# Kernel tuning notes

Measured on AMD Instinct MI355X. Metric: run time of the kernel, lower is better.

## Reference

```python
import jax, jax.numpy as jnp
import numpy as np

NUM_HEADS = 8
KERNEL_SEARCH = 5  # local attention window
EPS = 1e-5


def _layernorm(x, g, b):
    m = jnp.mean(x, axis=-1, keepdims=True)
    v = jnp.var(x, axis=-1, keepdims=True)
    return (x - m) / jnp.sqrt(v + EPS) * g + b


def _unfold3(x):
    # x: [N, C, H, W] -> [N, C*9, H*W]; matches torch F.unfold(kernel=3, pad=1)
    # ordering: channel-major, kernel position (row-major) minor.
    N, C, H, W = x.shape
    xp = jnp.pad(x, ((0, 0), (0, 0), (1, 1), (1, 1)))
    pats = jnp.stack([xp[:, :, i:i + H, j:j + W] for i in range(3) for j in range(3)], axis=2)
    return pats.reshape(N, C * 9, H * W)


def _sai2token(x, w_mlp):
    # x: [b, c, a, h, w] -> tokens [h*w, b*a, spa_dim]
    b, c, a, h, w = x.shape
    x = x.transpose(0, 2, 1, 3, 4).reshape(b * a, c, h, w)
    tok = _unfold3(x).transpose(2, 0, 1)  # [hw, b*a, c*9]
    return jnp.einsum('lnk,ek->lne', tok, w_mlp)


def _local_mask(h, w, k):
    # additive mask [h*w, h*w]: 0 inside local kxk window, -inf outside
    kl, kr = k // 2, k - k // 2
    ii = jnp.arange(h)
    jj = jnp.arange(w)
    okh = (ii[None, :] >= ii[:, None] - kl) & (ii[None, :] < ii[:, None] + kr)  # [h,h]
    okw = (jj[None, :] >= jj[:, None] - kl) & (jj[None, :] < jj[:, None] + kr)  # [w,w]
    ok = okh[:, None, :, None] & okw[None, :, None, :]  # [h,w,h,w]
    ok = ok.reshape(h * w, h * w)
    return jnp.where(ok, 0.0, -jnp.inf).astype(jnp.float32)


def _attention(qk_in, v_in, in_proj_w, out_proj_w, bias):
    # qk_in/v_in: [L, B, E]; torch nn.MultiheadAttention, no biases, eval mode
    L, B, E = qk_in.shape
    Dh = E // NUM_HEADS
    Wq, Wk, Wv = in_proj_w[:E], in_proj_w[E:2 * E], in_proj_w[2 * E:]
    q = jnp.einsum('lbe,fe->lbf', qk_in, Wq).reshape(L, B, NUM_HEADS, Dh)
    k = jnp.einsum('lbe,fe->lbf', qk_in, Wk).reshape(L, B, NUM_HEADS, Dh)
    v = jnp.einsum('lbe,fe->lbf', v_in, Wv).reshape(L, B, NUM_HEADS, Dh)
    scale = 1.0 / np.sqrt(Dh).astype(np.float32)
    scores = jnp.einsum('lbhd,mbhd->bhlm', q, k) * scale + bias[None, None]
    attn = jax.nn.softmax(scores, axis=-1)
    out = jnp.einsum('bhlm,mbhd->lbhd', attn, v).reshape(L, B, E)
    return jnp.einsum('lbe,fe->lbf', out, out_proj_w)


def reference(buffer, spa_position, w_mlp, ln1_g, ln1_b, in_proj_w, out_proj_w,
              ln2_g, ln2_b, ff_w1, ff_w2, conv_w):
    b, c, a, h, w = buffer.shape
    bias = _local_mask(h, w, KERNEL_SEARCH)
    tok = _sai2token(buffer, w_mlp)          # [hw, b*a, E]
    pe = _sai2token(spa_position, w_mlp)
    x = _layernorm(tok + pe, ln1_g, ln1_b)
    tok = _attention(x, tok, in_proj_w, out_proj_w, bias) + tok
    # feed-forward (dropout is identity in eval)
    ff = _layernorm(tok, ln2_g, ln2_b)
    ff = jax.nn.relu(jnp.einsum('lbe,fe->lbf', ff, ff_w1))
    tok = jnp.einsum('lbf,ef->lbe', ff, ff_w2) + tok
    # Token2SAI: '(h w) (b a) e -> b e a h w' then 1x1x1 conv3d
    buf = tok.reshape(h, w, b, a, -1).transpose(2, 4, 3, 0, 1)  # [b, E, a, h, w]
    return jnp.einsum('oe,beahw->boahw', conv_w, buf)


def setup_inputs() -> dict:
    key = jax.random.key(0)
    ks = jax.random.split(key, 8)
    b, c, a, h, w = 1, 64, 25, 32, 32
    E = 2 * c
    s = 0.02
    return {
        'buffer': jax.random.normal(ks[0], (b, c, a, h, w), jnp.float32),
        'spa_position': jax.random.normal(ks[1], (b, c, a, h, w), jnp.float32),
        'w_mlp': jax.random.normal(ks[2], (E, c * 9), jnp.float32) * s,
        'ln1_g': jnp.ones((E,), jnp.float32),
        'ln1_b': jnp.zeros((E,), jnp.float32),
        'in_proj_w': jax.random.normal(ks[3], (3 * E, E), jnp.float32) * s,
        'out_proj_w': jax.random.normal(ks[4], (E, E), jnp.float32) * s,
        'ln2_g': jnp.ones((E,), jnp.float32),
        'ln2_b': jnp.zeros((E,), jnp.float32),
        'ff_w1': jax.random.normal(ks[5], (2 * E, E), jnp.float32) * s,
        'ff_w2': jax.random.normal(ks[6], (E, 2 * E), jnp.float32) * s,
        'conv_w': jax.random.normal(ks[7], (c, E), jnp.float32) * s,
    }
```

## Files before the change

### kernel.cpp

```cpp
#include <hip/hip_runtime.h>
#include <math.h>

#define Lh 32
#define Lw 32
#define LL 1024
#define BN 25
#define EE 128
#define CC 64
#define NHD 8
#define DH 16
#define FFD 256
#define MROWS 25600

typedef __attribute__((ext_vector_type(8))) short short8;
typedef __attribute__((ext_vector_type(4))) float f32x4;

__device__ inline ushort f2b(float x) {
    union { float f; unsigned u; } v; v.f = x;
    unsigned r = (v.u + 0x7fffu + ((v.u >> 16) & 1u)) >> 16;
    return (ushort)r;
}
__device__ inline float b2f(ushort u) {
    union { unsigned u; float f; } v; v.u = ((unsigned)u) << 16;
    return v.f;
}

#define OFF_W2  0
#define OFF_WQK 73728
#define OFF_WV  106496
#define OFF_WO  122880
#define OFF_W1  139264
#define OFF_W2F 172032
#define OFF_WC  204800
#define W_TOTAL 212992
#define PREPW_BLOCKS 832

__global__ __launch_bounds__(256) void k_prep(
    const float* __restrict__ w_mlp, const float* __restrict__ in_proj,
    const float* __restrict__ out_proj, const float* __restrict__ ff_w1,
    const float* __restrict__ ff_w2, const float* __restrict__ conv_w,
    const float* __restrict__ buf, const float* __restrict__ spa,
    ushort* __restrict__ Wb, ushort* __restrict__ T, ushort* __restrict__ S)
{
    __shared__ float t0[64][33];
    __shared__ float t1[64][33];
    const int t = threadIdx.x;
    if (blockIdx.x < PREPW_BLOCKS) {
        int i = blockIdx.x * 256 + t;
        if (i >= W_TOTAL) return;
        if (i < 73728) {
            int e = i / 576, k = i - e * 576;
            int tap = k >> 6, ch = k & 63;
            Wb[OFF_W2 + i] = f2b(w_mlp[e * 576 + ch * 9 + tap]);
            return;
        }
        i -= 73728;
        if (i < 32768) {
            float v = in_proj[i];
            Wb[OFF_WQK + i] = f2b(i < 16384 ? v * 0.25f : v);
            return;
        }
        i -= 32768;
        if (i < 16384) { Wb[OFF_WV + i] = f2b(in_proj[32768 + i]); return; }
        i -= 16384;
        if (i < 16384) {
            int e = i >> 7, kpos = i & 127;
            int c = kpos >> 5, q = (kpos >> 3) & 3, ii = kpos & 7;
            int orig = (2 * c + (ii >> 2)) * 16 + q * 4 + (ii & 3);
            Wb[OFF_WO + i] = f2b(out_proj[e * 128 + orig]);
            return;
        }
        i -= 16384;
        if (i < 32768) { Wb[OFF_W1 + i] = f2b(ff_w1[i]); return; }
        i -= 32768;
        if (i < 32768) {
            int e = i >> 8, kpos = i & 255;
            int c = kpos >> 5, q = (kpos >> 3) & 3, ii = kpos & 7;
            int orig = (2 * c + (ii >> 2)) * 16 + q * 4 + (ii & 3);
            Wb[OFF_W2F + i] = f2b(ff_w2[e * 256 + orig]);
            return;
        }
        i -= 32768;
        {
            int o = i >> 7, kpos = i & 127;
            int c = kpos >> 5, q = (kpos >> 3) & 3, ii = kpos & 7;
            int orig = (2 * c + (ii >> 2)) * 16 + q * 4 + (ii & 3);
            Wb[OFF_WC + i] = f2b(conv_w[o * 128 + orig]);
        }
        return;
    }
    const int bid = blockIdx.x - PREPW_BLOCKS;
    const int n = bid >> 5, y = bid & 31;
    {
        int ch = t >> 2, x8 = (t & 3) * 8;
        const float* p = buf + ((size_t)(ch * BN + n) * LL + y * Lw + x8);
        const float* q = spa + ((size_t)(ch * BN + n) * LL + y * Lw + x8);
        float4 a0 = ((const float4*)p)[0], a1 = ((const float4*)p)[1];
        float4 b0 = ((const float4*)q)[0], b1 = ((const float4*)q)[1];
        float* d0 = &t0[ch][x8];
        float* d1 = &t1[ch][x8];
        d0[0] = a0.x; d0[1] = a0.y; d0[2] = a0.z; d0[3] = a0.w;
        d0[4] = a1.x; d0[5] = a1.y; d0[6] = a1.z; d0[7] = a1.w;
        d1[0] = a0.x + b0.x; d1[1] = a0.y + b0.y; d1[2] = a0.z + b0.z; d1[3] = a0.w + b0.w;
        d1[4] = a1.x + b1.x; d1[5] = a1.y + b1.y; d1[6] = a1.z + b1.z; d1[7] = a1.w + b1.w;
    }
    __syncthreads();
    {
        int x = t >> 3, c8 = (t & 7) * 8;
        union { ushort u[8]; uint4 v; } o0, o1;
#pragma unroll
        for (int j = 0; j < 8; j++) { o0.u[j] = f2b(t0[c8 + j][x]); o1.u[j] = f2b(t1[c8 + j][x]); }
        size_t base = (((size_t)n * Lh + y) * Lw + x) * 64 + c8;
        *(uint4*)(T + base) = o0.v;
        *(uint4*)(S + base) = o1.v;
    }
}

__global__ __launch_bounds__(256) void k_tok_qkv(
    const ushort* __restrict__ T, const ushort* __restrict__ S,
    const ushort* __restrict__ W2, const ushort* __restrict__ WQK,
    const ushort* __restrict__ WV, const float* __restrict__ g1,
    const float* __restrict__ b1, ushort* __restrict__ TOKb,
    ushort* __restrict__ Qh, ushort* __restrict__ Kh, ushort* __restrict__ VTg)
{
    const int bid = blockIdx.x;
    const int idx = (bid & 7) * 100 + (bid >> 3);
    const int n = idx / 32, y = idx & 31;
    __shared__ ushort At[3 * 34 * 72];
    __shared__ ushort As_[3 * 34 * 72];
    __shared__ ushort Xs[32 * 136];
    __shared__ ushort Vs[32 * 136];
    __shared__ float2 red[32][4];
    const int t = threadIdx.x;
    const uint4 z = make_uint4(0, 0, 0, 0);

    {
        int x = t >> 3, c8 = (t & 7) * 8;
#pragma unroll
        for (int dy = 0; dy < 3; dy++) {
            int yy = y + dy - 1;
            uint4 va = z, vs = z;
            if (yy >= 0 && yy < Lh) {
                size_t gi = (((size_t)n * Lh + yy) * Lw + x) * 64 + c8;
                va = *(const uint4*)(T + gi);
                vs = *(const uint4*)(S + gi);
            }
            *(uint4*)(At + (dy * 34 + x + 1) * 72 + c8) = va;
            *(uint4*)(As_ + (dy * 34 + x + 1) * 72 + c8) = vs;
        }
        if (t < 48) {
            int dy = t / 16, rem = t % 16;
            int colp = (rem >> 3) * 33, c8p = (rem & 7) * 8;
            *(uint4*)(At + (dy * 34 + colp) * 72 + c8p) = z;
            *(uint4*)(As_ + (dy * 34 + colp) * 72 + c8p) = z;
        }
    }
    __syncthreads();

    const int w = t >> 6, lane = t & 63;
    const int col = lane & 15, quad = lane >> 4;
    f32x4 accT[2][2] = {}, accS[2][2] = {};

    for (int tap = 0; tap < 9; tap++) {
        int dy = tap / 3, dx = tap % 3;
#pragma unroll
        for (int cc = 0; cc < 2; cc++) {
            int kg = tap * 64 + cc * 32 + quad * 8;
            short8 b0 = *(const short8*)(W2 + (size_t)(w * 32 + col) * 576 + kg);
            short8 bq = *(const short8*)(W2 + (size_t)(w * 32 + 16 + col) * 576 + kg);
            int abase = (dy * 34 + col + dx) * 72 + cc * 32 + quad * 8;
            short8 aT0 = *(const short8*)(At + abase);
            short8 aT1 = *(const short8*)(At + abase + 16 * 72);
            short8 aS0 = *(const short8*)(As_ + abase);
            short8 aS1 = *(const short8*)(As_ + abase + 16 * 72);
            accT[0][0] = __builtin_amdgcn_mfma_f32_16x16x32_bf16(aT0, b0, accT[0][0], 0, 0, 0);
            accT[0][1] = __builtin_amdgcn_mfma_f32_16x16x32_bf16(aT0, bq, accT[0][1], 0, 0, 0);
            accT[1][0] = __builtin_amdgcn_mfma_f32_16x16x32_bf16(aT1, b0, accT[1][0], 0, 0, 0);
            accT[1][1] = __builtin_amdgcn_mfma_f32_16x16x32_bf16(aT1, bq, accT[1][1], 0, 0, 0);
            accS[0][0] = __builtin_amdgcn_mfma_f32_16x16x32_bf16(aS0, b0, accS[0][0], 0, 0, 0);
            accS[0][1] = __builtin_amdgcn_mfma_f32_16x16x32_bf16(aS0, bq, accS[0][1], 0, 0, 0);
            accS[1][0] = __builtin_amdgcn_mfma_f32_16x16x32_bf16(aS1, b0, accS[1][0], 0, 0, 0);
            accS[1][1] = __builtin_amdgcn_mfma_f32_16x16x32_bf16(aS1, bq, accS[1][1], 0, 0, 0);
        }
    }

#pragma unroll
    for (int mi = 0; mi < 2; mi++)
#pragma unroll
        for (int r = 0; r < 4; r++) {
            float a0 = accS[mi][0][r], a1 = accS[mi][1][r];
            float ss = a0 + a1, qq = a0 * a0 + a1 * a1;
#pragma unroll
            for (int m = 1; m < 16; m <<= 1) {
                ss += __shfl_xor(ss, m, 64);
                qq += __shfl_xor(qq, m, 64);
            }
            if (col == 0) red[mi * 16 + quad * 4 + r][w] = make_float2(ss, qq);
        }
    __syncthreads();

    const float ga = g1[w * 32 + col],      ba = b1[w * 32 + col];
    const float gb = g1[w * 32 + 16 + col], bb = b1[w * 32 + 16 + col];
#pragma unroll
    for (int mi = 0; mi < 2; mi++)
#pragma unroll
        for (int r = 0; r < 4; r++) {
            int x = mi * 16 + quad * 4 + r;
            float2 p0 = red[x][0], p1 = red[x][1], p2 = red[x][2], p3 = red[x][3];
            float mean = (p0.x + p1.x + p2.x + p3.x) * (1.f / 128.f);
            float var  = (p0.y + p1.y + p2.y + p3.y) * (1.f / 128.f) - mean * mean;
            float rstd = rsqrtf(var + 1e-5f);
            int e0 = w * 32 + col, e1 = w * 32 + 16 + col;
            Xs[x * 136 + e0] = f2b((accS[mi][0][r] - mean) * rstd * ga + ba);
            Xs[x * 136 + e1] = f2b((accS[mi][1][r] - mean) * rstd * gb + bb);
            Vs[x * 136 + e0] = f2b(accT[mi][0][r]);
            Vs[x * 136 + e1] = f2b(accT[mi][1][r]);
        }
    __syncthreads();

    short8 xb[2][4], xv[2][4];
#pragma unroll
    for (int j = 0; j < 2; j++)
#pragma unroll
        for (int kc = 0; kc < 4; kc++) {
            xb[j][kc] = *(const short8*)(Xs + (j * 16 + col) * 136 + kc * 32 + quad * 8);
            xv[j][kc] = *(const short8*)(Vs + (j * 16 + col) * 136 + kc * 32 + quad * 8);
        }
    f32x4 Q[2][2] = {}, K[2][2] = {}, V[2][2] = {};
#pragma unroll
    for (int hj = 0; hj < 2; hj++) {
        int h = 2 * w + hj;
#pragma unroll
        for (int kc = 0; kc < 4; kc++) {
            short8 aq = *(const short8*)(WQK + (size_t)(h * 16 + col) * 128 + kc * 32 + quad * 8);
            short8 ak = *(const short8*)(WQK + (size_t)(128 + h * 16 + col) * 128 + kc * 32 + quad * 8);
            short8 av = *(const short8*)(WV + (size_t)(h * 16 + col) * 128 + kc * 32 + quad * 8);
#pragma unroll
            for (int j = 0; j < 2; j++) {
                Q[hj][j] = __builtin_amdgcn_mfma_f32_16x16x32_bf16(aq, xb[j][kc], Q[hj][j], 0, 0, 0);
                K[hj][j] = __builtin_amdgcn_mfma_f32_16x16x32_bf16(ak, xb[j][kc], K[hj][j], 0, 0, 0);
                V[hj][j] = __builtin_amdgcn_mfma_f32_16x16x32_bf16(av, xv[j][kc], V[hj][j], 0, 0, 0);
            }
        }
    }
    ushort* VTs = At;
#pragma unroll
    for (int hj = 0; hj < 2; hj++) {
        int h = 2 * w + hj;
#pragma unroll
        for (int j = 0; j < 2; j++) {
            int l = y * 32 + j * 16 + col;
            size_t base = ((size_t)(n * 8 + h) * 1024 + l) * 16 + quad * 4;
            ushort4 oq, ok;
            oq.x = f2b(Q[hj][j][0]); oq.y = f2b(Q[hj][j][1]); oq.z = f2b(Q[hj][j][2]); oq.w = f2b(Q[hj][j][3]);
            ok.x = f2b(K[hj][j][0]); ok.y = f2b(K[hj][j][1]); ok.z = f2b(K[hj][j][2]); ok.w = f2b(K[hj][j][3]);
            *(ushort4*)(Qh + base) = oq;
            *(ushort4*)(Kh + base) = ok;
            int xp = ((col >> 2) << 3) + (j << 2) + (col & 3);
#pragma unroll
            for (int r = 0; r < 4; r++)
                VTs[(h * 16 + quad * 4 + r) * 34 + xp] = f2b(V[hj][j][r]);
        }
    }
#pragma unroll
    for (int k = 0; k < 2; k++) {
        int idx2 = t + k * 256;
        int r = idx2 >> 4, seg = idx2 & 15;
        *(uint4*)(TOKb + ((size_t)((y * 32 + r) * 25 + n)) * 128 + seg * 8) =
            *(const uint4*)(Vs + r * 136 + seg * 8);
    }
    __syncthreads();
    {
        int h = t >> 5, rem = t & 31, d = rem >> 1, xh = (rem & 1) * 16;
        size_t vrow = ((size_t)(n * 8 + h) * 32 + y) * 512;
        union { ushort u[8]; uint4 v; } o0, o1;
#pragma unroll
        for (int j = 0; j < 8; j++) {
            o0.u[j] = VTs[(h * 16 + d) * 34 + xh + j];
            o1.u[j] = VTs[(h * 16 + d) * 34 + xh + 8 + j];
        }
        *(uint4*)(VTg + vrow + d * 32 + xh)     = o0.v;
        *(uint4*)(VTg + vrow + d * 32 + xh + 8) = o1.v;
    }
}

__global__ __launch_bounds__(256) void k_attn_ffn(
    const ushort* __restrict__ Qh, const ushort* __restrict__ Kh,
    const ushort* __restrict__ VTg, const ushort* __restrict__ WOP,
    const float* __restrict__ g2, const float* __restrict__ b2,
    const ushort* __restrict__ W1, const ushort* __restrict__ W2P,
    const ushort* __restrict__ WCP, const ushort* __restrict__ TOKb,
    float* __restrict__ out)
{
    __shared__ ushort OX[16 * 136];
    __shared__ ushort Rs[16 * 136];
    __shared__ ushort Hs[16 * 264];
    __shared__ ushort Ys[16 * 136];
    __shared__ float2 red[16][4];
    const int bid = blockIdx.x;
    const int idx = (bid & 7) * 200 + (bid >> 3);
    const int n = idx / 64, rem = idx & 63;
    const int y = rem >> 1, half = rem & 1;
    const int l0 = y * 32 + half * 16;
    const int t = threadIdx.x, w = t >> 6, lane = t & 63;
    const int col = lane & 15, quad = lane >> 4;

    {
        int r = t >> 4, seg = t & 15;
        *(uint4*)(Rs + r * 136 + seg * 8) =
            *(const uint4*)(TOKb + ((size_t)((l0 + r) * 25 + n)) * 128 + seg * 8);
    }

    short8 z8 = {0, 0, 0, 0, 0, 0, 0, 0};
    const int qx = half * 16 + col;
    f32x4 O2[2] = {};
#pragma unroll
    for (int hj = 0; hj < 2; hj++) {
        const int h = 2 * w + hj;
        const size_t base = (size_t)(n * 8 + h) * 1024;
        const size_t vbase = ((size_t)(n * 8 + h) * 32) * 512;

        short8 qf = z8;
        if (quad < 2)
            qf = *(const short8*)(Qh + (base + y * 32 + half * 16 + col) * 16 + quad * 8);

        f32x4 Sc[10] = {};
#pragma unroll
        for (int tt = 0; tt < 10; tt++) {
            int kr = tt >> 1, kx = ((tt & 1) << 4) + col;
            int yyc = min(max(y - 2 + kr, 0), 31);
            short8 kf = z8;
            if (quad < 2)
                kf = *(const short8*)(Kh + (base + yyc * 32 + kx) * 16 + quad * 8);
            Sc[tt] = __builtin_amdgcn_mfma_f32_16x16x32_bf16(kf, qf, Sc[tt], 0, 0, 0);
        }

        float mx = -1e30f;
#pragma unroll
        for (int tt = 0; tt < 10; tt++) {
            int yy = y - 2 + (tt >> 1);
            bool rok = (yy >= 0) && (yy < 32);
            int kxb = ((tt & 1) << 4) + quad * 4;
#pragma unroll
            for (int r = 0; r < 4; r++) {
                int dd = kxb + r - qx;
                bool ok = rok && ((unsigned)(dd + 2) <= 4u);
                float v = ok ? Sc[tt][r] : -1e30f;
                Sc[tt][r] = v;
                mx = fmaxf(mx, v);
            }
        }
        mx = fmaxf(mx, __shfl_xor(mx, 16, 64));
        mx = fmaxf(mx, __shfl_xor(mx, 32, 64));
        float sum = 0.f;
#pragma unroll
        for (int tt = 0; tt < 10; tt++)
#pragma unroll
            for (int r = 0; r < 4; r++) {
                float p = __expf(Sc[tt][r] - mx);
                Sc[tt][r] = p;
                sum += p;
            }
        sum += __shfl_xor(sum, 16, 64);
        sum += __shfl_xor(sum, 32, 64);
        const float inv = 1.f / sum;

#pragma unroll
        for (int c = 0; c < 5; c++) {
            int yyc = min(max(y - 2 + c, 0), 31);
            short8 vt = *(const short8*)(VTg + vbase + (size_t)yyc * 512 + col * 32 + quad * 8);
            union { ushort u[8]; short8 s; } pb;
#pragma unroll
            for (int i = 0; i < 8; i++)
                pb.u[i] = f2b(Sc[2 * c + (i >> 2)][i & 3] * inv);
            O2[hj] = __builtin_amdgcn_mfma_f32_16x16x32_bf16(vt, pb.s, O2[hj], 0, 0, 0);
        }
    }

    {
        union { ushort u[8]; uint4 v; } pb;
#pragma unroll
        for (int i = 0; i < 8; i++)
            pb.u[i] = f2b(O2[i >> 2][i & 3]);
        *(uint4*)(OX + col * 136 + w * 32 + quad * 8) = pb.v;
    }
    __syncthreads();

    f32x4 Y[2] = {};
#pragma unroll
    for (int kc = 0; kc < 4; kc++) {
        short8 hb = *(const short8*)(OX + col * 136 + kc * 32 + quad * 8);
#pragma unroll
        for (int jj = 0; jj < 2; jj++) {
            int et = 2 * w + jj;
            short8 a = *(const short8*)(WOP + (size_t)(et * 16 + col) * 128 + kc * 32 + quad * 8);
            Y[jj] = __builtin_amdgcn_mfma_f32_16x16x32_bf16(a, hb, Y[jj], 0, 0, 0);
        }
    }
    float sum = 0.f, sq = 0.f;
#pragma unroll
    for (int jj = 0; jj < 2; jj++)
#pragma unroll
        for (int r = 0; r < 4; r++) {
            int e = (2 * w + jj) * 16 + quad * 4 + r;
            float v = Y[jj][r] + b2f(Rs[col * 136 + e]);
            Y[jj][r] = v;
            sum += v; sq += v * v;
        }
    sum += __shfl_xor(sum, 16, 64); sum += __shfl_xor(sum, 32, 64);
    sq  += __shfl_xor(sq, 16, 64);  sq  += __shfl_xor(sq, 32, 64);
    if (quad == 0) red[col][w] = make_float2(sum, sq);
    __syncthreads();

    {
        float2 p0 = red[col][0], p1 = red[col][1], p2 = red[col][2], p3 = red[col][3];
        float mean = (p0.x + p1.x + p2.x + p3.x) * (1.f / 128.f);
        float var  = (p0.y + p1.y + p2.y + p3.y) * (1.f / 128.f) - mean * mean;
        float rstd = rsqrtf(var + 1e-5f);
#pragma unroll
        for (int jj = 0; jj < 2; jj++)
#pragma unroll
            for (int r = 0; r < 4; r++) {
                int e = (2 * w + jj) * 16 + quad * 4 + r;
                OX[col * 136 + e] = f2b((Y[jj][r] - mean) * rstd * g2[e] + b2[e]);
            }
    }
    __syncthreads();

    short8 xb[4];
#pragma unroll
    for (int kc = 0; kc < 4; kc++)
        xb[kc] = *(const short8*)(OX + col * 136 + kc * 32 + quad * 8);
    f32x4 H[4] = {};
#pragma unroll
    for (int j = 0; j < 4; j++) {
        int ft = 4 * w + j;
#pragma unroll
        for (int kc = 0; kc < 4; kc++) {
            short8 a = *(const short8*)(W1 + (size_t)(ft * 16 + col) * 128 + kc * 32 + quad * 8);
            H[j] = __builtin_amdgcn_mfma_f32_16x16x32_bf16(a, xb[kc], H[j], 0, 0, 0);
        }
    }
#pragma unroll
    for (int cc = 0; cc < 2; cc++) {
        union { ushort u[8]; uint4 v; } pb;
#pragma unroll
        for (int i = 0; i < 8; i++)
            pb.u[i] = f2b(fmaxf(H[2 * cc + (i >> 2)][i & 3], 0.f));
        *(uint4*)(Hs + col * 264 + (2 * w + cc) * 32 + quad * 8) = pb.v;
    }
    __syncthreads();

    f32x4 Y2[2] = {};
#pragma unroll
    for (int kc = 0; kc < 8; kc++) {
        short8 hb = *(const short8*)(Hs + col * 264 + kc * 32 + quad * 8);
#pragma unroll
        for (int j = 0; j < 2; j++) {
            int et = 2 * w + j;
            short8 a = *(const short8*)(W2P + (size_t)(et * 16 + col) * 256 + kc * 32 + quad * 8);
            Y2[j] = __builtin_amdgcn_mfma_f32_16x16x32_bf16(a, hb, Y2[j], 0, 0, 0);
        }
    }
    {
        union { ushort u[8]; uint4 v; } pb;
#pragma unroll
        for (int i = 0; i < 8; i++)
            pb.u[i] = f2b(Y2[i >> 2][i & 3] + Y[i >> 2][i & 3]);
        *(uint4*)(Ys + col * 136 + w * 32 + quad * 8) = pb.v;
    }
    __syncthreads();

    f32x4 O = {};
#pragma unroll
    for (int c = 0; c < 4; c++) {
        short8 yb = *(const short8*)(Ys + col * 136 + c * 32 + quad * 8);
        short8 a = *(const short8*)(WCP + (size_t)(w * 16 + col) * 128 + c * 32 + quad * 8);
        O = __builtin_amdgcn_mfma_f32_16x16x32_bf16(a, yb, O, 0, 0, 0);
    }
    const int l = l0 + col;
#pragma unroll
    for (int r2 = 0; r2 < 4; r2++) {
        int o = w * 16 + quad * 4 + r2;
        out[(size_t)(o * 25 + n) * 1024 + l] = O[r2];
    }
}

extern "C" void kernel_launch(void* const* d_in, const int* in_sizes, int n_in,
                              void* d_out, int out_size, void* d_ws, size_t ws_size,
                              hipStream_t stream)
{
    const float* buffer   = (const float*)d_in[0];
    const float* spa      = (const float*)d_in[1];
    const float* w_mlp    = (const float*)d_in[2];
    const float* ln1_g    = (const float*)d_in[3];
    const float* ln1_b    = (const float*)d_in[4];
    const float* in_proj  = (const float*)d_in[5];
    const float* out_proj = (const float*)d_in[6];
    const float* ln2_g    = (const float*)d_in[7];
    const float* ln2_b    = (const float*)d_in[8];
    const float* ff_w1    = (const float*)d_in[9];
    const float* ff_w2    = (const float*)d_in[10];
    const float* conv_w   = (const float*)d_in[11];
    float* out = (float*)d_out;

    char* ws = (char*)d_ws;
    ushort* TOKb = (ushort*)(ws);
    ushort* Qh   = (ushort*)(ws + 6553600);
    ushort* Kh   = (ushort*)(ws + 13107200);
    ushort* VTg  = (ushort*)(ws + 19660800);
    ushort* Tbf  = (ushort*)(ws + 26214400);
    ushort* Sbf  = (ushort*)(ws + 29491200);
    ushort* Wb   = (ushort*)(ws + 32768000);

    k_prep<<<dim3(PREPW_BLOCKS + 800), 256, 0, stream>>>(
        w_mlp, in_proj, out_proj, ff_w1, ff_w2, conv_w,
        buffer, spa, Wb, Tbf, Sbf);
    k_tok_qkv<<<dim3(800), 256, 0, stream>>>(Tbf, Sbf, Wb + OFF_W2,
                                             Wb + OFF_WQK, Wb + OFF_WV,
                                             ln1_g, ln1_b, TOKb, Qh, Kh, VTg);
    k_attn_ffn<<<dim3(1600), 256, 0, stream>>>(Qh, Kh, VTg, Wb + OFF_WO,
                                               ln2_g, ln2_b, Wb + OFF_W1,
                                               Wb + OFF_W2F, Wb + OFF_WC,
                                               TOKb, out);
}
```

Measured before the change: 176.2 us.

## Split fused attention+FFN kernel into separate attention and out-proj/FFN kernels

Splits the fused local-attention-plus-FFN kernel into two launches. Attention output goes to a new global bf16 buffer, which the second kernel reads directly for the out-projection, LayerNorm and FFN. The attention kernel also precomputes the window mask as a bitmask and applies the softmax normalization once after the PV MFMA instead of scaling every probability. The intent is lower register/LDS pressure and better occupancy in each kernel, at the cost of an extra launch and a global round-trip of the attention output.

```diff
diff --git a/kernel.cpp b/kernel.cpp
--- a/kernel.cpp
+++ b/kernel.cpp
@@ -284,9 +284,103 @@
     }
 }
 
-__global__ __launch_bounds__(256) void k_attn_ffn(
+__global__ __launch_bounds__(256) void k_attn(
     const ushort* __restrict__ Qh, const ushort* __restrict__ Kh,
-    const ushort* __restrict__ VTg, const ushort* __restrict__ WOP,
+    const ushort* __restrict__ VTg, ushort* __restrict__ AOp)
+{
+    const int bid = blockIdx.x;
+    const int idx = (bid & 7) * 200 + (bid >> 3);
+    const int n = idx / 64, rem = idx & 63;
+    const int y = rem >> 1, half = rem & 1;
+    const int t = threadIdx.x, w = t >> 6, lane = t & 63;
+    const int col = lane & 15, quad = lane >> 4;
+    const int qx = half * 16 + col;
+
+    unsigned long long mbits = 0;
+#pragma unroll
+    for (int tt = 0; tt < 10; tt++) {
+        int yy = y - 2 + (tt >> 1);
+        bool rok = (yy >= 0) && (yy < 32);
+        int kxb = ((tt & 1) << 4) + quad * 4;
+#pragma unroll
+        for (int r = 0; r < 4; r++) {
+            int dd = kxb + r - qx;
+            if (rok && ((unsigned)(dd + 2) <= 4u))
+                mbits |= 1ull << (tt * 4 + r);
+        }
+    }
+
+    short8 z8 = {0, 0, 0, 0, 0, 0, 0, 0};
+    f32x4 O2[2] = {};
+#pragma unroll
+    for (int hj = 0; hj < 2; hj++) {
+        const int h = 2 * w + hj;
+        const size_t base = (size_t)(n * 8 + h) * 1024;
+        const size_t vbase = ((size_t)(n * 8 + h) * 32) * 512;
+
+        short8 qf = z8;
+        if (quad < 2)
+            qf = *(const short8*)(Qh + (base + y * 32 + half * 16 + col) * 16 + quad * 8);
+
+        f32x4 Sc[10] = {};
+#pragma unroll
+        for (int tt = 0; tt < 10; tt++) {
+            int kr = tt >> 1, kx = ((tt & 1) << 4) + col;
+            int yyc = min(max(y - 2 + kr, 0), 31);
+            short8 kf = z8;
+            if (quad < 2)
+                kf = *(const short8*)(Kh + (base + yyc * 32 + kx) * 16 + quad * 8);
+            Sc[tt] = __builtin_amdgcn_mfma_f32_16x16x32_bf16(kf, qf, Sc[tt], 0, 0, 0);
+        }
+
+        float mx = -1e30f;
+#pragma unroll
+        for (int tt = 0; tt < 10; tt++)
+#pragma unroll
+            for (int r = 0; r < 4; r++) {
+                bool ok = (mbits >> (tt * 4 + r)) & 1;
+                float v = ok ? Sc[tt][r] : -1e30f;
+                Sc[tt][r] = v;
+                mx = fmaxf(mx, v);
+            }
+        mx = fmaxf(mx, __shfl_xor(mx, 16, 64));
+        mx = fmaxf(mx, __shfl_xor(mx, 32, 64));
+        float sum = 0.f;
+#pragma unroll
+        for (int tt = 0; tt < 10; tt++)
+#pragma unroll
+            for (int r = 0; r < 4; r++) {
+                float p = __expf(Sc[tt][r] - mx);
+                Sc[tt][r] = p;
+                sum += p;
+            }
+        sum += __shfl_xor(sum, 16, 64);
+        sum += __shfl_xor(sum, 32, 64);
+        const float inv = 1.f / sum;
+
+#pragma unroll
+        for (int c = 0; c < 5; c++) {
+            int yyc = min(max(y - 2 + c, 0), 31);
+            short8 vt = *(const short8*)(VTg + vbase + (size_t)yyc * 512 + col * 32 + quad * 8);
+            union { ushort u[8]; short8 s; } pb;
+#pragma unroll
+            for (int i = 0; i < 8; i++)
+                pb.u[i] = f2b(Sc[2 * c + (i >> 2)][i & 3]);
+            O2[hj] = __builtin_amdgcn_mfma_f32_16x16x32_bf16(vt, pb.s, O2[hj], 0, 0, 0);
+        }
+#pragma unroll
+        for (int r = 0; r < 4; r++) O2[hj][r] *= inv;
+    }
+
+    union { ushort u[8]; uint4 v; } pb;
+#pragma unroll
+    for (int i = 0; i < 8; i++)
+        pb.u[i] = f2b(O2[i >> 2][i & 3]);
+    *(uint4*)(AOp + ((size_t)(n * 1024 + y * 32 + half * 16 + col)) * 128 + w * 32 + quad * 8) = pb.v;
+}
+
+__global__ __launch_bounds__(256) void k_oln_ffn(
+    const ushort* __restrict__ AOp, const ushort* __restrict__ WOP,
     const float* __restrict__ g2, const float* __restrict__ b2,
     const ushort* __restrict__ W1, const ushort* __restrict__ W2P,
     const ushort* __restrict__ WCP, const ushort* __restrict__ TOKb,
@@ -310,86 +404,12 @@
         *(uint4*)(Rs + r * 136 + seg * 8) =
             *(const uint4*)(TOKb + ((size_t)((l0 + r) * 25 + n)) * 128 + seg * 8);
     }
-
-    short8 z8 = {0, 0, 0, 0, 0, 0, 0, 0};
-    const int qx = half * 16 + col;
-    f32x4 O2[2] = {};
-#pragma unroll
-    for (int hj = 0; hj < 2; hj++) {
-        const int h = 2 * w + hj;
-        const size_t base = (size_t)(n * 8 + h) * 1024;
-        const size_t vbase = ((size_t)(n * 8 + h) * 32) * 512;
-
-        short8 qf = z8;
-        if (quad < 2)
-            qf = *(const short8*)(Qh + (base + y * 32 + half * 16 + col) * 16 + quad * 8);
-
-        f32x4 Sc[10] = {};
-#pragma unroll
-        for (int tt = 0; tt < 10; tt++) {
-            int kr = tt >> 1, kx = ((tt & 1) << 4) + col;
-            int yyc = min(max(y - 2 + kr, 0), 31);
-            short8 kf = z8;
-            if (quad < 2)
-                kf = *(const short8*)(Kh + (base + yyc * 32 + kx) * 16 + quad * 8);
-            Sc[tt] = __builtin_amdgcn_mfma_f32_16x16x32_bf16(kf, qf, Sc[tt], 0, 0, 0);
-        }
-
-        float mx = -1e30f;
-#pragma unroll
-        for (int tt = 0; tt < 10; tt++) {
-            int yy = y - 2 + (tt >> 1);
-            bool rok = (yy >= 0) && (yy < 32);
-            int kxb = ((tt & 1) << 4) + quad * 4;
-#pragma unroll
-            for (int r = 0; r < 4; r++) {
-                int dd = kxb + r - qx;
-                bool ok = rok && ((unsigned)(dd + 2) <= 4u);
-                float v = ok ? Sc[tt][r] : -1e30f;
-                Sc[tt][r] = v;
-                mx = fmaxf(mx, v);
-            }
-        }
-        mx = fmaxf(mx, __shfl_xor(mx, 16, 64));
-        mx = fmaxf(mx, __shfl_xor(mx, 32, 64));
-        float sum = 0.f;
-#pragma unroll
-        for (int tt = 0; tt < 10; tt++)
-#pragma unroll
-            for (int r = 0; r < 4; r++) {
-                float p = __expf(Sc[tt][r] - mx);
-                Sc[tt][r] = p;
-                sum += p;
-            }
-        sum += __shfl_xor(sum, 16, 64);
-        sum += __shfl_xor(sum, 32, 64);
-        const float inv = 1.f / sum;
-
-#pragma unroll
-        for (int c = 0; c < 5; c++) {
-            int yyc = min(max(y - 2 + c, 0), 31);
-            short8 vt = *(const short8*)(VTg + vbase + (size_t)yyc * 512 + col * 32 + quad * 8);
-            union { ushort u[8]; short8 s; } pb;
-#pragma unroll
-            for (int i = 0; i < 8; i++)
-                pb.u[i] = f2b(Sc[2 * c + (i >> 2)][i & 3] * inv);
-            O2[hj] = __builtin_amdgcn_mfma_f32_16x16x32_bf16(vt, pb.s, O2[hj], 0, 0, 0);
-        }
-    }
-
-    {
-        union { ushort u[8]; uint4 v; } pb;
-#pragma unroll
-        for (int i = 0; i < 8; i++)
-            pb.u[i] = f2b(O2[i >> 2][i & 3]);
-        *(uint4*)(OX + col * 136 + w * 32 + quad * 8) = pb.v;
-    }
     __syncthreads();
 
     f32x4 Y[2] = {};
 #pragma unroll
     for (int kc = 0; kc < 4; kc++) {
-        short8 hb = *(const short8*)(OX + col * 136 + kc * 32 + quad * 8);
+        short8 hb = *(const short8*)(AOp + ((size_t)(n * 1024 + l0 + col)) * 128 + kc * 32 + quad * 8);
 #pragma unroll
         for (int jj = 0; jj < 2; jj++) {
             int et = 2 * w + jj;
@@ -509,9 +529,10 @@
     ushort* Qh   = (ushort*)(ws + 6553600);
     ushort* Kh   = (ushort*)(ws + 13107200);
     ushort* VTg  = (ushort*)(ws + 19660800);
-    ushort* Tbf  = (ushort*)(ws + 26214400);
-    ushort* Sbf  = (ushort*)(ws + 29491200);
-    ushort* Wb   = (ushort*)(ws + 32768000);
+    ushort* AOp  = (ushort*)(ws + 26214400);
+    ushort* Tbf  = (ushort*)(ws + 32768000);
+    ushort* Sbf  = (ushort*)(ws + 36044800);
+    ushort* Wb   = (ushort*)(ws + 39321600);
 
     k_prep<<<dim3(PREPW_BLOCKS + 800), 256, 0, stream>>>(
         w_mlp, in_proj, out_proj, ff_w1, ff_w2, conv_w,
@@ -519,8 +540,8 @@
     k_tok_qkv<<<dim3(800), 256, 0, stream>>>(Tbf, Sbf, Wb + OFF_W2,
                                              Wb + OFF_WQK, Wb + OFF_WV,
                                              ln1_g, ln1_b, TOKb, Qh, Kh, VTg);
-    k_attn_ffn<<<dim3(1600), 256, 0, stream>>>(Qh, Kh, VTg, Wb + OFF_WO,
-                                               ln2_g, ln2_b, Wb + OFF_W1,
-                                               Wb + OFF_W2F, Wb + OFF_WC,
-                                               TOKb, out);
-}
+    k_attn<<<dim3(1600), 256, 0, stream>>>(Qh, Kh, VTg, AOp);
+    k_oln_ffn<<<dim3(1600), 256, 0, stream>>>(AOp, Wb + OFF_WO, ln2_g, ln2_b,
+                                              Wb + OFF_W1, Wb + OFF_W2F,
+                                              Wb + OFF_WC, TOKb, out);
+}
```

New measurement: 183.7 us. +4.3%, slower.

## Fuse input transpose/bf16 conversion into token kernel and defer softmax normalization

Applied to the files above, without the earlier changes.

The fp32 input transpose and bf16 conversion now happen inside the token/QKV kernel, which reads the three needed rows of buffer and spa directly and no longer uses intermediate T/S bf16 arrays. This removes the global round trip for those arrays, but each input row is now read and transposed three times, once per neighbouring output row, with extra syncs. In attention, the local-window mask is precomputed once as a bitmask outside the head loop. Softmax normalization is applied to the accumulated output instead of to each probability, which slightly changes bf16 rounding.

```diff
diff --git a/kernel.cpp b/kernel.cpp
--- a/kernel.cpp
+++ b/kernel.cpp
@@ -33,91 +33,58 @@
 #define OFF_W2F 172032
 #define OFF_WC  204800
 #define W_TOTAL 212992
-#define PREPW_BLOCKS 832
 
 __global__ __launch_bounds__(256) void k_prep(
     const float* __restrict__ w_mlp, const float* __restrict__ in_proj,
     const float* __restrict__ out_proj, const float* __restrict__ ff_w1,
     const float* __restrict__ ff_w2, const float* __restrict__ conv_w,
+    ushort* __restrict__ Wb)
+{
+    int i = blockIdx.x * 256 + threadIdx.x;
+    if (i >= W_TOTAL) return;
+    if (i < 73728) {
+        int e = i / 576, k = i - e * 576;
+        int tap = k >> 6, ch = k & 63;
+        Wb[OFF_W2 + i] = f2b(w_mlp[e * 576 + ch * 9 + tap]);
+        return;
+    }
+    i -= 73728;
+    if (i < 32768) {
+        float v = in_proj[i];
+        Wb[OFF_WQK + i] = f2b(i < 16384 ? v * 0.25f : v);
+        return;
+    }
+    i -= 32768;
+    if (i < 16384) { Wb[OFF_WV + i] = f2b(in_proj[32768 + i]); return; }
+    i -= 16384;
+    if (i < 16384) {
+        int e = i >> 7, kpos = i & 127;
+        int c = kpos >> 5, q = (kpos >> 3) & 3, ii = kpos & 7;
+        int orig = (2 * c + (ii >> 2)) * 16 + q * 4 + (ii & 3);
+        Wb[OFF_WO + i] = f2b(out_proj[e * 128 + orig]);
+        return;
+    }
+    i -= 16384;
+    if (i < 32768) { Wb[OFF_W1 + i] = f2b(ff_w1[i]); return; }
+    i -= 32768;
+    if (i < 32768) {
+        int e = i >> 8, kpos = i & 255;
+        int c = kpos >> 5, q = (kpos >> 3) & 3, ii = kpos & 7;
+        int orig = (2 * c + (ii >> 2)) * 16 + q * 4 + (ii & 3);
+        Wb[OFF_W2F + i] = f2b(ff_w2[e * 256 + orig]);
+        return;
+    }
+    i -= 32768;
+    {
+        int o = i >> 7, kpos = i & 127;
+        int c = kpos >> 5, q = (kpos >> 3) & 3, ii = kpos & 7;
+        int orig = (2 * c + (ii >> 2)) * 16 + q * 4 + (ii & 3);
+        Wb[OFF_WC + i] = f2b(conv_w[o * 128 + orig]);
+    }
+}
+
+__global__ __launch_bounds__(256) void k_tok_qkv(
     const float* __restrict__ buf, const float* __restrict__ spa,
-    ushort* __restrict__ Wb, ushort* __restrict__ T, ushort* __restrict__ S)
-{
-    __shared__ float t0[64][33];
-    __shared__ float t1[64][33];
-    const int t = threadIdx.x;
-    if (blockIdx.x < PREPW_BLOCKS) {
-        int i = blockIdx.x * 256 + t;
-        if (i >= W_TOTAL) return;
-        if (i < 73728) {
-            int e = i / 576, k = i - e * 576;
-            int tap = k >> 6, ch = k & 63;
-            Wb[OFF_W2 + i] = f2b(w_mlp[e * 576 + ch * 9 + tap]);
-            return;
-        }
-        i -= 73728;
-        if (i < 32768) {
-            float v = in_proj[i];
-            Wb[OFF_WQK + i] = f2b(i < 16384 ? v * 0.25f : v);
-            return;
-        }
-        i -= 32768;
-        if (i < 16384) { Wb[OFF_WV + i] = f2b(in_proj[32768 + i]); return; }
-        i -= 16384;
-        if (i < 16384) {
-            int e = i >> 7, kpos = i & 127;
-            int c = kpos >> 5, q = (kpos >> 3) & 3, ii = kpos & 7;
-            int orig = (2 * c + (ii >> 2)) * 16 + q * 4 + (ii & 3);
-            Wb[OFF_WO + i] = f2b(out_proj[e * 128 + orig]);
-            return;
-        }
-        i -= 16384;
-        if (i < 32768) { Wb[OFF_W1 + i] = f2b(ff_w1[i]); return; }
-        i -= 32768;
-        if (i < 32768) {
-            int e = i >> 8, kpos = i & 255;
-            int c = kpos >> 5, q = (kpos >> 3) & 3, ii = kpos & 7;
-            int orig = (2 * c + (ii >> 2)) * 16 + q * 4 + (ii & 3);
-            Wb[OFF_W2F + i] = f2b(ff_w2[e * 256 + orig]);
-            return;
-        }
-        i -= 32768;
-        {
-            int o = i >> 7, kpos = i & 127;
-            int c = kpos >> 5, q = (kpos >> 3) & 3, ii = kpos & 7;
-            int orig = (2 * c + (ii >> 2)) * 16 + q * 4 + (ii & 3);
-            Wb[OFF_WC + i] = f2b(conv_w[o * 128 + orig]);
-        }
-        return;
-    }
-    const int bid = blockIdx.x - PREPW_BLOCKS;
-    const int n = bid >> 5, y = bid & 31;
-    {
-        int ch = t >> 2, x8 = (t & 3) * 8;
-        const float* p = buf + ((size_t)(ch * BN + n) * LL + y * Lw + x8);
-        const float* q = spa + ((size_t)(ch * BN + n) * LL + y * Lw + x8);
-        float4 a0 = ((const float4*)p)[0], a1 = ((const float4*)p)[1];
-        float4 b0 = ((const float4*)q)[0], b1 = ((const float4*)q)[1];
-        float* d0 = &t0[ch][x8];
-        float* d1 = &t1[ch][x8];
-        d0[0] = a0.x; d0[1] = a0.y; d0[2] = a0.z; d0[3] = a0.w;
-        d0[4] = a1.x; d0[5] = a1.y; d0[6] = a1.z; d0[7] = a1.w;
-        d1[0] = a0.x + b0.x; d1[1] = a0.y + b0.y; d1[2] = a0.z + b0.z; d1[3] = a0.w + b0.w;
-        d1[4] = a1.x + b1.x; d1[5] = a1.y + b1.y; d1[6] = a1.z + b1.z; d1[7] = a1.w + b1.w;
-    }
-    __syncthreads();
-    {
-        int x = t >> 3, c8 = (t & 7) * 8;
-        union { ushort u[8]; uint4 v; } o0, o1;
-#pragma unroll
-        for (int j = 0; j < 8; j++) { o0.u[j] = f2b(t0[c8 + j][x]); o1.u[j] = f2b(t1[c8 + j][x]); }
-        size_t base = (((size_t)n * Lh + y) * Lw + x) * 64 + c8;
-        *(uint4*)(T + base) = o0.v;
-        *(uint4*)(S + base) = o1.v;
-    }
-}
-
-__global__ __launch_bounds__(256) void k_tok_qkv(
-    const ushort* __restrict__ T, const ushort* __restrict__ S,
     const ushort* __restrict__ W2, const ushort* __restrict__ WQK,
     const ushort* __restrict__ WV, const float* __restrict__ g1,
     const float* __restrict__ b1, ushort* __restrict__ TOKb,
@@ -131,29 +98,51 @@
     __shared__ ushort Xs[32 * 136];
     __shared__ ushort Vs[32 * 136];
     __shared__ float2 red[32][4];
+    float* t0 = (float*)Xs;
+    float* t1 = (float*)Vs;
     const int t = threadIdx.x;
     const uint4 z = make_uint4(0, 0, 0, 0);
 
-    {
-        int x = t >> 3, c8 = (t & 7) * 8;
-#pragma unroll
-        for (int dy = 0; dy < 3; dy++) {
-            int yy = y + dy - 1;
-            uint4 va = z, vs = z;
-            if (yy >= 0 && yy < Lh) {
-                size_t gi = (((size_t)n * Lh + yy) * Lw + x) * 64 + c8;
-                va = *(const uint4*)(T + gi);
-                vs = *(const uint4*)(S + gi);
-            }
-            *(uint4*)(At + (dy * 34 + x + 1) * 72 + c8) = va;
-            *(uint4*)(As_ + (dy * 34 + x + 1) * 72 + c8) = vs;
-        }
-        if (t < 48) {
-            int dy = t / 16, rem = t % 16;
-            int colp = (rem >> 3) * 33, c8p = (rem & 7) * 8;
-            *(uint4*)(At + (dy * 34 + colp) * 72 + c8p) = z;
-            *(uint4*)(As_ + (dy * 34 + colp) * 72 + c8p) = z;
-        }
+    for (int dy = 0; dy < 3; dy++) {
+        int yy = y + dy - 1;
+        if (yy >= 0 && yy < Lh) {
+            {
+                int ch = t >> 2, x8 = (t & 3) * 8;
+                const float* p = buf + ((size_t)(ch * BN + n) * LL + yy * Lw + x8);
+                const float* q = spa + ((size_t)(ch * BN + n) * LL + yy * Lw + x8);
+                float4 a0 = ((const float4*)p)[0], a1 = ((const float4*)p)[1];
+                float4 b0 = ((const float4*)q)[0], b1 = ((const float4*)q)[1];
+                float* d0 = t0 + ch * 33 + x8;
+                float* d1 = t1 + ch * 33 + x8;
+                d0[0] = a0.x; d0[1] = a0.y; d0[2] = a0.z; d0[3] = a0.w;
+                d0[4] = a1.x; d0[5] = a1.y; d0[6] = a1.z; d0[7] = a1.w;
+                d1[0] = a0.x + b0.x; d1[1] = a0.y + b0.y; d1[2] = a0.z + b0.z; d1[3] = a0.w + b0.w;
+                d1[4] = a1.x + b1.x; d1[5] = a1.y + b1.y; d1[6] = a1.z + b1.z; d1[7] = a1.w + b1.w;
+            }
+            __syncthreads();
+            {
+                int x = t >> 3, c8 = (t & 7) * 8;
+                union { ushort u[8]; uint4 v; } o0, o1;
+#pragma unroll
+                for (int j = 0; j < 8; j++) {
+                    o0.u[j] = f2b(t0[(c8 + j) * 33 + x]);
+                    o1.u[j] = f2b(t1[(c8 + j) * 33 + x]);
+                }
+                *(uint4*)(At + (dy * 34 + x + 1) * 72 + c8) = o0.v;
+                *(uint4*)(As_ + (dy * 34 + x + 1) * 72 + c8) = o1.v;
+            }
+            __syncthreads();
+        } else {
+            int x = t >> 3, c8 = (t & 7) * 8;
+            *(uint4*)(At + (dy * 34 + x + 1) * 72 + c8) = z;
+            *(uint4*)(As_ + (dy * 34 + x + 1) * 72 + c8) = z;
+        }
+    }
+    if (t < 48) {
+        int dy = t / 16, rem = t % 16;
+        int colp = (rem >> 3) * 33, c8p = (rem & 7) * 8;
+        *(uint4*)(At + (dy * 34 + colp) * 72 + c8p) = z;
+        *(uint4*)(As_ + (dy * 34 + colp) * 72 + c8p) = z;
     }
     __syncthreads();
 
@@ -304,6 +293,7 @@
     const int l0 = y * 32 + half * 16;
     const int t = threadIdx.x, w = t >> 6, lane = t & 63;
     const int col = lane & 15, quad = lane >> 4;
+    const int qx = half * 16 + col;
 
     {
         int r = t >> 4, seg = t & 15;
@@ -311,8 +301,21 @@
             *(const uint4*)(TOKb + ((size_t)((l0 + r) * 25 + n)) * 128 + seg * 8);
     }
 
+    unsigned long long mbits = 0;
+#pragma unroll
+    for (int tt = 0; tt < 10; tt++) {
+        int yy = y - 2 + (tt >> 1);
+        bool rok = (yy >= 0) && (yy < 32);
+        int kxb = ((tt & 1) << 4) + quad * 4;
+#pragma unroll
+        for (int r = 0; r < 4; r++) {
+            int dd = kxb + r - qx;
+            if (rok && ((unsigned)(dd + 2) <= 4u))
+                mbits |= 1ull << (tt * 4 + r);
+        }
+    }
+
     short8 z8 = {0, 0, 0, 0, 0, 0, 0, 0};
-    const int qx = half * 16 + col;
     f32x4 O2[2] = {};
 #pragma unroll
     for (int hj = 0; hj < 2; hj++) {
@@ -337,19 +340,14 @@
 
         float mx = -1e30f;
 #pragma unroll
-        for (int tt = 0; tt < 10; tt++) {
-            int yy = y - 2 + (tt >> 1);
-            bool rok = (yy >= 0) && (yy < 32);
-            int kxb = ((tt & 1) << 4) + quad * 4;
+        for (int tt = 0; tt < 10; tt++)
 #pragma unroll
             for (int r = 0; r < 4; r++) {
-                int dd = kxb + r - qx;
-                bool ok = rok && ((unsigned)(dd + 2) <= 4u);
+                bool ok = (mbits >> (tt * 4 + r)) & 1;
                 float v = ok ? Sc[tt][r] : -1e30f;
                 Sc[tt][r] = v;
                 mx = fmaxf(mx, v);
             }
-        }
         mx = fmaxf(mx, __shfl_xor(mx, 16, 64));
         mx = fmaxf(mx, __shfl_xor(mx, 32, 64));
         float sum = 0.f;
@@ -372,9 +370,11 @@
             union { ushort u[8]; short8 s; } pb;
 #pragma unroll
             for (int i = 0; i < 8; i++)
-                pb.u[i] = f2b(Sc[2 * c + (i >> 2)][i & 3] * inv);
+                pb.u[i] = f2b(Sc[2 * c + (i >> 2)][i & 3]);
             O2[hj] = __builtin_amdgcn_mfma_f32_16x16x32_bf16(vt, pb.s, O2[hj], 0, 0, 0);
         }
+#pragma unroll
+        for (int r = 0; r < 4; r++) O2[hj][r] *= inv;
     }
 
     {
@@ -509,14 +509,11 @@
     ushort* Qh   = (ushort*)(ws + 6553600);
     ushort* Kh   = (ushort*)(ws + 13107200);
     ushort* VTg  = (ushort*)(ws + 19660800);
-    ushort* Tbf  = (ushort*)(ws + 26214400);
-    ushort* Sbf  = (ushort*)(ws + 29491200);
-    ushort* Wb   = (ushort*)(ws + 32768000);
-
-    k_prep<<<dim3(PREPW_BLOCKS + 800), 256, 0, stream>>>(
-        w_mlp, in_proj, out_proj, ff_w1, ff_w2, conv_w,
-        buffer, spa, Wb, Tbf, Sbf);
-    k_tok_qkv<<<dim3(800), 256, 0, stream>>>(Tbf, Sbf, Wb + OFF_W2,
+    ushort* Wb   = (ushort*)(ws + 26214400);
+
+    k_prep<<<dim3((W_TOTAL + 255) / 256), 256, 0, stream>>>(
+        w_mlp, in_proj, out_proj, ff_w1, ff_w2, conv_w, Wb);
+    k_tok_qkv<<<dim3(800), 256, 0, stream>>>(buffer, spa, Wb + OFF_W2,
                                              Wb + OFF_WQK, Wb + OFF_WV,
                                              ln1_g, ln1_b, TOKb, Qh, Kh, VTg);
     k_attn_ffn<<<dim3(1600), 256, 0, stream>>>(Qh, Kh, VTg, Wb + OFF_WO,
```

Result: no change. 174.5 us (-1.0%).
